# Performance work log

Measured on AMD Instinct MI355X. Metric: run time of the kernel, lower is better.

## Reference

```python
import jax, jax.numpy as jnp
import numpy as np

EPS = 0.05  # blend weight of K_Rectify smoothing


def k_rectify(x_nbc, distance, idx, eps=EPS):
    """Distance-weighted neighbor smoothing.
    x_nbc: (N, B, C); distance, idx: (B, N, K). Returns (N, B, C)."""
    x_bnc = jnp.transpose(x_nbc, (1, 0, 2))                       # (B,N,C)
    B = x_bnc.shape[0]
    neigh = x_bnc[jnp.arange(B)[:, None, None], idx]              # (B,N,K,C) gather
    w = jax.nn.softmax(-distance, axis=-1)                        # closer -> larger weight
    smoothed = jnp.einsum('bnk,bnkc->bnc', w, neigh)              # (B,N,C)
    y = (1.0 - eps) * x_bnc + eps * smoothed
    return jnp.transpose(y, (1, 0, 2))


def monarch_linear(x, w1, w2, bias):
    """Monarch block-diagonal butterfly multiply on the last dim.
    w1: (k,q,p), w2: (l,s,r) with k*p == n, l*r == k*q."""
    shp = x.shape
    k, q, p = w1.shape
    l, s, r = w2.shape
    xb = x.reshape(-1, k, p)
    o1 = jnp.einsum('kqp,bkp->bkq', w1, xb)                       # (B*, k, q)
    o1 = o1.reshape(-1, r, l).transpose(0, 2, 1)                  # 'b (r l) -> b l r'
    o2 = jnp.einsum('lsr,blr->bls', w2, o1)                       # (B*, l, s)
    out = o2.transpose(0, 2, 1).reshape(-1, s * l) + bias         # 'b l s -> b (s l)'
    return out.reshape(*shp[:-1], s * l)


def setup_inputs() -> dict:
    key = jax.random.key(0)
    B, N, C, K, nblocks = 8, 8192, 256, 8, 8
    blk = C // nblocks
    ks = jax.random.split(key, 6)
    x = jax.random.normal(ks[0], (B, N, C), dtype=jnp.float32)
    distance = jax.random.uniform(ks[1], (B, N, K), dtype=jnp.float32)
    idx = jax.random.randint(ks[2], (B, N, K), 0, N)
    rf = jax.random.normal(ks[3], (B, N, C), dtype=jnp.float32)
    scale = 1.0 / np.sqrt(blk)
    w1 = jax.random.normal(ks[4], (nblocks, blk, blk), dtype=jnp.float32) * scale
    w2 = jax.random.normal(ks[5], (nblocks, blk, blk), dtype=jnp.float32) * scale
    bias = jnp.zeros((C,), dtype=jnp.float32)
    return {"x": x, "distance": distance, "idx": idx, "rf": rf,
            "w1": w1, "w2": w2, "bias": bias}


def reference(x, distance, idx, rf, w1, w2, bias):
    # _prepare_in: (B,N,C) -> (N,B,C)
    xs = jnp.transpose(x, (1, 0, 2))
    s1 = k_rectify(xs, distance, idx)            # smooth_in
    t = monarch_linear(s1, w1, w2, bias)         # Monarch block-diag matmul
    s2 = k_rectify(t, distance, idx)             # smooth_out
    return jnp.transpose(s2, (1, 0, 2)) + rf     # _out_transform residual
```

## Files before the change

kernel.cpp:

```cpp
#include <hip/hip_runtime.h>

#define NPTS 8192
#define CH   256
#define KNB  8
#define NROWS 65536
#define ROWS_PER_BLK 32
#define ROWS_PER_IT  4
#define NIT (ROWS_PER_BLK / ROWS_PER_IT)
#define FT_STRIDE 36

#define NBLK_CONV 8192
#define NBLK_S1   (NROWS / ROWS_PER_BLK)
#define NBLK_S2   (NROWS / 16)

typedef unsigned short ushort_t;
typedef float  f32x4  __attribute__((ext_vector_type(4)));

#define BARRIER_LDS() do { \
    asm volatile("s_waitcnt lgkmcnt(0)" ::: "memory"); \
    __builtin_amdgcn_s_barrier(); \
} while (0)

__device__ __forceinline__ int xcd_swz(int h, int cpx) {
    return (h & 7) * cpx + (h >> 3);
}

__device__ __forceinline__ ushort_t f32_to_bf16(float f) {
    unsigned int b = __float_as_uint(f);
    b += 0x7FFFu + ((b >> 16) & 1u);
    return (ushort_t)(b >> 16);
}
__device__ __forceinline__ float bf16_to_f32(ushort_t u) {
    return __uint_as_float(((unsigned int)u) << 16);
}
__device__ __forceinline__ unsigned int pack_bf16(float lo, float hi) {
    return (unsigned int)f32_to_bf16(lo) | ((unsigned int)f32_to_bf16(hi) << 16);
}

__global__ __launch_bounds__(256) void pm_conv(
    const f32x4* __restrict__ x, uint4* __restrict__ xb)
{
    const int l = xcd_swz(blockIdx.x, NBLK_CONV / 8);
    const size_t i = (size_t)l * 256 + threadIdx.x;
    const f32x4 a = __builtin_nontemporal_load(&x[2 * i]);
    const f32x4 c = __builtin_nontemporal_load(&x[2 * i + 1]);
    uint4 o;
    o.x = pack_bf16(a.x, a.y);
    o.y = pack_bf16(a.z, a.w);
    o.z = pack_bf16(c.x, c.y);
    o.w = pack_bf16(c.z, c.w);
    xb[i] = o;
}

__global__ __launch_bounds__(256, 4) void pm_stage1(
    const ushort_t* __restrict__ xb, const float* __restrict__ dist,
    const int* __restrict__ idx, const float* __restrict__ w1,
    const float* __restrict__ w2, const float* __restrict__ bias,
    ushort_t* __restrict__ t)
{
    const int c = threadIdx.x;

    __shared__ float s1[ROWS_PER_IT][CH];
    __shared__ float fT[ROWS_PER_IT][8 * FT_STRIDE];

    float4 w1r[8], w2r[8];
    {
        const float4* w1p = (const float4*)(w1 + c * 32);
        const float4* w2p = (const float4*)(w2 + ((c & 7) * 32 + (c >> 3)) * 32);
#pragma unroll
        for (int i = 0; i < 8; ++i) { w1r[i] = w1p[i]; w2r[i] = w2p[i]; }
    }
    const float bb = bias[c];
    const int l2   = c & 7;
    const int kb   = c >> 5;
    const int ftw  = l2 * FT_STRIDE + (c >> 3);

    const int rr   = __builtin_amdgcn_readfirstlane(threadIdx.x >> 6);
    const int lane = threadIdx.x & 63;

    const int lb       = xcd_swz(blockIdx.x, NBLK_S1 / 8);
    const int row_base = lb * ROWS_PER_BLK;
    const int b = row_base >> 13;
    const char* xbase  = (const char*)(xb + (size_t)b * NPTS * CH);
    const int laneoff  = lane * 8;

    float dcur[KNB]; int nbs[KNB];
    {
        const int row = row_base + rr;
        const float4 d0 = *(const float4*)(dist + (size_t)row * KNB);
        const float4 d1 = *(const float4*)(dist + (size_t)row * KNB + 4);
        const int4   i0 = *(const int4*)(idx + (size_t)row * KNB);
        const int4   i1 = *(const int4*)(idx + (size_t)row * KNB + 4);
        dcur[0]=d0.x; dcur[1]=d0.y; dcur[2]=d0.z; dcur[3]=d0.w;
        dcur[4]=d1.x; dcur[5]=d1.y; dcur[6]=d1.z; dcur[7]=d1.w;
        nbs[0]=__builtin_amdgcn_readfirstlane(i0.x);
        nbs[1]=__builtin_amdgcn_readfirstlane(i0.y);
        nbs[2]=__builtin_amdgcn_readfirstlane(i0.z);
        nbs[3]=__builtin_amdgcn_readfirstlane(i0.w);
        nbs[4]=__builtin_amdgcn_readfirstlane(i1.x);
        nbs[5]=__builtin_amdgcn_readfirstlane(i1.y);
        nbs[6]=__builtin_amdgcn_readfirstlane(i1.z);
        nbs[7]=__builtin_amdgcn_readfirstlane(i1.w);
    }
    ushort4 c0, g[KNB];
    {
        const int rloc = (row_base + rr) & (NPTS - 1);
        c0 = *(const ushort4*)(xbase + ((size_t)rloc << 9) + laneoff);
#pragma unroll
        for (int k = 0; k < KNB; ++k)
            g[k] = *(const ushort4*)(xbase + ((size_t)(unsigned)nbs[k] << 9) + laneoff);
    }

    for (int it = 0; it < NIT; ++it) {
        const bool more = (it + 1 < NIT);
        const int rown  = row_base + (more ? it + 1 : it) * ROWS_PER_IT + rr;

        const float4 dn0 = *(const float4*)(dist + (size_t)rown * KNB);
        const float4 dn1 = *(const float4*)(dist + (size_t)rown * KNB + 4);
        const int4   in0 = *(const int4*)(idx + (size_t)rown * KNB);
        const int4   in1 = *(const int4*)(idx + (size_t)rown * KNB + 4);

        float mn = dcur[0];
#pragma unroll
        for (int k = 1; k < KNB; ++k) mn = fminf(mn, dcur[k]);
        float e[KNB]; float sum = 0.f;
#pragma unroll
        for (int k = 0; k < KNB; ++k) { e[k] = __expf(mn - dcur[k]); sum += e[k]; }
        const float inv = 0.05f / sum;

        float4 acc;
        acc.x = 0.95f * bf16_to_f32(c0.x);
        acc.y = 0.95f * bf16_to_f32(c0.y);
        acc.z = 0.95f * bf16_to_f32(c0.z);
        acc.w = 0.95f * bf16_to_f32(c0.w);
#pragma unroll
        for (int k = 0; k < KNB; ++k) {
            const float w = e[k] * inv;
            acc.x += w * bf16_to_f32(g[k].x);
            acc.y += w * bf16_to_f32(g[k].y);
            acc.z += w * bf16_to_f32(g[k].z);
            acc.w += w * bf16_to_f32(g[k].w);
        }
        ((float4*)&s1[rr][0])[lane] = acc;

        BARRIER_LDS();

#pragma unroll
        for (int r2 = 0; r2 < ROWS_PER_IT; ++r2) {
            const float4* sb = (const float4*)(&s1[r2][kb * 32]);
            float a = 0.f;
#pragma unroll
            for (int p4 = 0; p4 < 8; ++p4) {
                const float4 s = sb[p4];
                a += w1r[p4].x * s.x + w1r[p4].y * s.y
                   + w1r[p4].z * s.z + w1r[p4].w * s.w;
            }
            fT[r2][ftw] = a;
        }

        if (more) {
            dcur[0]=dn0.x; dcur[1]=dn0.y; dcur[2]=dn0.z; dcur[3]=dn0.w;
            dcur[4]=dn1.x; dcur[5]=dn1.y; dcur[6]=dn1.z; dcur[7]=dn1.w;
            nbs[0]=__builtin_amdgcn_readfirstlane(in0.x);
            nbs[1]=__builtin_amdgcn_readfirstlane(in0.y);
            nbs[2]=__builtin_amdgcn_readfirstlane(in0.z);
            nbs[3]=__builtin_amdgcn_readfirstlane(in0.w);
            nbs[4]=__builtin_amdgcn_readfirstlane(in1.x);
            nbs[5]=__builtin_amdgcn_readfirstlane(in1.y);
            nbs[6]=__builtin_amdgcn_readfirstlane(in1.z);
            nbs[7]=__builtin_amdgcn_readfirstlane(in1.w);
            const int rloc = rown & (NPTS - 1);
            c0 = *(const ushort4*)(xbase + ((size_t)rloc << 9) + laneoff);
#pragma unroll
            for (int k = 0; k < KNB; ++k)
                g[k] = *(const ushort4*)(xbase + ((size_t)(unsigned)nbs[k] << 9) + laneoff);
        }

        BARRIER_LDS();

#pragma unroll
        for (int r2 = 0; r2 < ROWS_PER_IT; ++r2) {
            const float4* fp = (const float4*)(&fT[r2][l2 * FT_STRIDE]);
            float a = bb;
#pragma unroll
            for (int r4 = 0; r4 < 8; ++r4) {
                const float4 f = fp[r4];
                a += w2r[r4].x * f.x + w2r[r4].y * f.y
                   + w2r[r4].z * f.z + w2r[r4].w * f.w;
            }
            __builtin_nontemporal_store(
                f32_to_bf16(a),
                &t[(size_t)(row_base + it * ROWS_PER_IT + r2) * CH + c]);
        }
    }
}

__global__ __launch_bounds__(256, 4) void pm_stage2(
    const ushort_t* __restrict__ t, const float* __restrict__ dist,
    const int* __restrict__ idx, const float* __restrict__ rf,
    float* __restrict__ out)
{
    const int w     = __builtin_amdgcn_readfirstlane(threadIdx.x >> 6);
    const int lane  = threadIdx.x & 63;
    const int lb    = xcd_swz(blockIdx.x, NBLK_S2 / 8);
    const int wrow0 = lb * 16 + w * 4;
    const int b     = wrow0 >> 13;
    const char* tbase = (const char*)(t + (size_t)b * NPTS * CH);
    const int laneoff = lane * 8;

    int   nbs[4][KNB];
    float d [4][KNB];
#pragma unroll
    for (int r = 0; r < 4; ++r) {
        const int row = wrow0 + r;
        const float4 d0 = *(const float4*)(dist + (size_t)row * KNB);
        const float4 d1 = *(const float4*)(dist + (size_t)row * KNB + 4);
        const int4   i0 = *(const int4*)(idx + (size_t)row * KNB);
        const int4   i1 = *(const int4*)(idx + (size_t)row * KNB + 4);
        d[r][0]=d0.x; d[r][1]=d0.y; d[r][2]=d0.z; d[r][3]=d0.w;
        d[r][4]=d1.x; d[r][5]=d1.y; d[r][6]=d1.z; d[r][7]=d1.w;
        nbs[r][0]=__builtin_amdgcn_readfirstlane(i0.x);
        nbs[r][1]=__builtin_amdgcn_readfirstlane(i0.y);
        nbs[r][2]=__builtin_amdgcn_readfirstlane(i0.z);
        nbs[r][3]=__builtin_amdgcn_readfirstlane(i0.w);
        nbs[r][4]=__builtin_amdgcn_readfirstlane(i1.x);
        nbs[r][5]=__builtin_amdgcn_readfirstlane(i1.y);
        nbs[r][6]=__builtin_amdgcn_readfirstlane(i1.z);
        nbs[r][7]=__builtin_amdgcn_readfirstlane(i1.w);
    }

    ushort4 c0[4], g[4][KNB];
    f32x4   rv[4];
#pragma unroll
    for (int r = 0; r < 4; ++r) {
        const int rloc = (wrow0 + r) & (NPTS - 1);
        c0[r] = *(const ushort4*)(tbase + ((size_t)rloc << 9) + laneoff);
        rv[r] = __builtin_nontemporal_load(
                    &((const f32x4*)rf)[(size_t)(wrow0 + r) * 64 + lane]);
#pragma unroll
        for (int k = 0; k < KNB; ++k)
            g[r][k] = *(const ushort4*)(tbase + ((size_t)(unsigned)nbs[r][k] << 9) + laneoff);
    }

#pragma unroll
    for (int r = 0; r < 4; ++r) {
        float mn = d[r][0];
#pragma unroll
        for (int k = 1; k < KNB; ++k) mn = fminf(mn, d[r][k]);
        float e[KNB]; float sum = 0.f;
#pragma unroll
        for (int k = 0; k < KNB; ++k) { e[k] = __expf(mn - d[r][k]); sum += e[k]; }
        const float inv = 0.05f / sum;

        f32x4 acc;
        acc.x = 0.95f * bf16_to_f32(c0[r].x) + rv[r].x;
        acc.y = 0.95f * bf16_to_f32(c0[r].y) + rv[r].y;
        acc.z = 0.95f * bf16_to_f32(c0[r].z) + rv[r].z;
        acc.w = 0.95f * bf16_to_f32(c0[r].w) + rv[r].w;
#pragma unroll
        for (int k = 0; k < KNB; ++k) {
            const float wk = e[k] * inv;
            acc.x += wk * bf16_to_f32(g[r][k].x);
            acc.y += wk * bf16_to_f32(g[r][k].y);
            acc.z += wk * bf16_to_f32(g[r][k].z);
            acc.w += wk * bf16_to_f32(g[r][k].w);
        }
        __builtin_nontemporal_store(
            acc, &((f32x4*)out)[(size_t)(wrow0 + r) * 64 + lane]);
    }
}

extern "C" void kernel_launch(void* const* d_in, const int* in_sizes, int n_in,
                              void* d_out, int out_size, void* d_ws, size_t ws_size,
                              hipStream_t stream) {
    const float* x    = (const float*)d_in[0];
    const float* dist = (const float*)d_in[1];
    const int*   idx  = (const int*)d_in[2];
    const float* rf   = (const float*)d_in[3];
    const float* w1   = (const float*)d_in[4];
    const float* w2   = (const float*)d_in[5];
    const float* bias = (const float*)d_in[6];
    float* out = (float*)d_out;

    ushort_t* t  = (ushort_t*)d_ws;
    ushort_t* xb = (ushort_t*)((char*)d_ws + (size_t)NROWS * CH * 2);

    pm_conv  <<<NBLK_CONV, 256, 0, stream>>>((const f32x4*)x, (uint4*)xb);
    pm_stage1<<<NBLK_S1,   256, 0, stream>>>(xb, dist, idx, w1, w2, bias, t);
    pm_stage2<<<NBLK_S2,   256, 0, stream>>>(t, dist, idx, rf, out);
}
```

Measured before the change: 267.0 us.

## Batch stage1 into 16-row phases with double-buffered gathers and transient weight registers

Stage1 now handles 16 rows per barrier phase instead of 4. Two gather buffers are interleaved so neighbour loads for upcoming rows are in flight while the current rows are blended. The Monarch weights are reloaded into registers per phase instead of being held for the whole kernel, which frees VGPRs for the extra in-flight gathers. This cuts barrier count and raises memory-level parallelism, at the cost of repeated weight loads from cache, more LDS, and possible register pressure. The stage2 blend is also rewritten with vector arithmetic.

```diff
diff --git a/kernel.cpp b/kernel.cpp
--- a/kernel.cpp
+++ b/kernel.cpp
@@ -5,8 +5,7 @@
 #define KNB  8
 #define NROWS 65536
 #define ROWS_PER_BLK 32
-#define ROWS_PER_IT  4
-#define NIT (ROWS_PER_BLK / ROWS_PER_IT)
+#define PHASE_ROWS 16
 #define FT_STRIDE 36
 
 #define NBLK_CONV 8192
@@ -35,6 +34,12 @@
 }
 __device__ __forceinline__ unsigned int pack_bf16(float lo, float hi) {
     return (unsigned int)f32_to_bf16(lo) | ((unsigned int)f32_to_bf16(hi) << 16);
+}
+__device__ __forceinline__ f32x4 bf4(ushort4 u) {
+    f32x4 r;
+    r.x = bf16_to_f32(u.x); r.y = bf16_to_f32(u.y);
+    r.z = bf16_to_f32(u.z); r.w = bf16_to_f32(u.w);
+    return r;
 }
 
 __global__ __launch_bounds__(256) void pm_conv(
@@ -60,16 +65,9 @@
 {
     const int c = threadIdx.x;
 
-    __shared__ float s1[ROWS_PER_IT][CH];
-    __shared__ float fT[ROWS_PER_IT][8 * FT_STRIDE];
-
-    float4 w1r[8], w2r[8];
-    {
-        const float4* w1p = (const float4*)(w1 + c * 32);
-        const float4* w2p = (const float4*)(w2 + ((c & 7) * 32 + (c >> 3)) * 32);
-#pragma unroll
-        for (int i = 0; i < 8; ++i) { w1r[i] = w1p[i]; w2r[i] = w2p[i]; }
-    }
+    __shared__ float s1[PHASE_ROWS][CH];
+    __shared__ float fT[PHASE_ROWS][8 * FT_STRIDE];
+
     const float bb = bias[c];
     const int l2   = c & 7;
     const int kb   = c >> 5;
@@ -84,115 +82,112 @@
     const char* xbase  = (const char*)(xb + (size_t)b * NPTS * CH);
     const int laneoff  = lane * 8;
 
-    float dcur[KNB]; int nbs[KNB];
-    {
-        const int row = row_base + rr;
-        const float4 d0 = *(const float4*)(dist + (size_t)row * KNB);
-        const float4 d1 = *(const float4*)(dist + (size_t)row * KNB + 4);
-        const int4   i0 = *(const int4*)(idx + (size_t)row * KNB);
-        const int4   i1 = *(const int4*)(idx + (size_t)row * KNB + 4);
-        dcur[0]=d0.x; dcur[1]=d0.y; dcur[2]=d0.z; dcur[3]=d0.w;
-        dcur[4]=d1.x; dcur[5]=d1.y; dcur[6]=d1.z; dcur[7]=d1.w;
-        nbs[0]=__builtin_amdgcn_readfirstlane(i0.x);
-        nbs[1]=__builtin_amdgcn_readfirstlane(i0.y);
-        nbs[2]=__builtin_amdgcn_readfirstlane(i0.z);
-        nbs[3]=__builtin_amdgcn_readfirstlane(i0.w);
-        nbs[4]=__builtin_amdgcn_readfirstlane(i1.x);
-        nbs[5]=__builtin_amdgcn_readfirstlane(i1.y);
-        nbs[6]=__builtin_amdgcn_readfirstlane(i1.z);
-        nbs[7]=__builtin_amdgcn_readfirstlane(i1.w);
-    }
-    ushort4 c0, g[KNB];
-    {
-        const int rloc = (row_base + rr) & (NPTS - 1);
-        c0 = *(const ushort4*)(xbase + ((size_t)rloc << 9) + laneoff);
-#pragma unroll
-        for (int k = 0; k < KNB; ++k)
-            g[k] = *(const ushort4*)(xbase + ((size_t)(unsigned)nbs[k] << 9) + laneoff);
-    }
-
-    for (int it = 0; it < NIT; ++it) {
-        const bool more = (it + 1 < NIT);
-        const int rown  = row_base + (more ? it + 1 : it) * ROWS_PER_IT + rr;
-
-        const float4 dn0 = *(const float4*)(dist + (size_t)rown * KNB);
-        const float4 dn1 = *(const float4*)(dist + (size_t)rown * KNB + 4);
-        const int4   in0 = *(const int4*)(idx + (size_t)rown * KNB);
-        const int4   in1 = *(const int4*)(idx + (size_t)rown * KNB + 4);
-
-        float mn = dcur[0];
-#pragma unroll
-        for (int k = 1; k < KNB; ++k) mn = fminf(mn, dcur[k]);
-        float e[KNB]; float sum = 0.f;
-#pragma unroll
-        for (int k = 0; k < KNB; ++k) { e[k] = __expf(mn - dcur[k]); sum += e[k]; }
-        const float inv = 0.05f / sum;
-
-        float4 acc;
-        acc.x = 0.95f * bf16_to_f32(c0.x);
-        acc.y = 0.95f * bf16_to_f32(c0.y);
-        acc.z = 0.95f * bf16_to_f32(c0.z);
-        acc.w = 0.95f * bf16_to_f32(c0.w);
-#pragma unroll
-        for (int k = 0; k < KNB; ++k) {
-            const float w = e[k] * inv;
-            acc.x += w * bf16_to_f32(g[k].x);
-            acc.y += w * bf16_to_f32(g[k].y);
-            acc.z += w * bf16_to_f32(g[k].z);
-            acc.w += w * bf16_to_f32(g[k].w);
-        }
-        ((float4*)&s1[rr][0])[lane] = acc;
+#define LOAD_META(dd, nn, row) do {                                        \
+    const float4 m0_ = *(const float4*)(dist + (size_t)(row) * KNB);       \
+    const float4 m1_ = *(const float4*)(dist + (size_t)(row) * KNB + 4);   \
+    const int4   j0_ = *(const int4*)(idx + (size_t)(row) * KNB);          \
+    const int4   j1_ = *(const int4*)(idx + (size_t)(row) * KNB + 4);      \
+    dd[0]=m0_.x; dd[1]=m0_.y; dd[2]=m0_.z; dd[3]=m0_.w;                    \
+    dd[4]=m1_.x; dd[5]=m1_.y; dd[6]=m1_.z; dd[7]=m1_.w;                    \
+    nn[0]=__builtin_amdgcn_readfirstlane(j0_.x);                           \
+    nn[1]=__builtin_amdgcn_readfirstlane(j0_.y);                           \
+    nn[2]=__builtin_amdgcn_readfirstlane(j0_.z);                           \
+    nn[3]=__builtin_amdgcn_readfirstlane(j0_.w);                           \
+    nn[4]=__builtin_amdgcn_readfirstlane(j1_.x);                           \
+    nn[5]=__builtin_amdgcn_readfirstlane(j1_.y);                           \
+    nn[6]=__builtin_amdgcn_readfirstlane(j1_.z);                           \
+    nn[7]=__builtin_amdgcn_readfirstlane(j1_.w);                           \
+} while (0)
+
+#define ISSUE_G(cc, gg, nn, row) do {                                      \
+    const int rloc_ = (row) & (NPTS - 1);                                  \
+    cc = *(const ushort4*)(xbase + ((size_t)rloc_ << 9) + laneoff);        \
+    _Pragma("unroll")                                                      \
+    for (int k_ = 0; k_ < KNB; ++k_)                                       \
+        gg[k_] = *(const ushort4*)(xbase + ((size_t)(unsigned)nn[k_] << 9) + laneoff); \
+} while (0)
+
+#define BLEND(cc, gg, dd, srow) do {                                       \
+    float mn_ = dd[0];                                                     \
+    _Pragma("unroll")                                                      \
+    for (int k_ = 1; k_ < KNB; ++k_) mn_ = fminf(mn_, dd[k_]);             \
+    float e_[KNB]; float sum_ = 0.f;                                       \
+    _Pragma("unroll")                                                      \
+    for (int k_ = 0; k_ < KNB; ++k_) { e_[k_] = __expf(mn_ - dd[k_]); sum_ += e_[k_]; } \
+    const float inv_ = 0.05f / sum_;                                       \
+    f32x4 acc_ = 0.95f * bf4(cc);                                          \
+    _Pragma("unroll")                                                      \
+    for (int k_ = 0; k_ < KNB; ++k_) acc_ += (e_[k_] * inv_) * bf4(gg[k_]); \
+    *(f32x4*)(&s1[srow][lane * 4]) = acc_;                                 \
+} while (0)
+
+    float dA[KNB], dB[KNB];
+    int   nA[KNB], nB[KNB];
+    ushort4 cA, gA[KNB], cB, gB[KNB];
+
+    LOAD_META(dA, nA, row_base + rr);
+    LOAD_META(dB, nB, row_base + 4 + rr);
+    ISSUE_G(cA, gA, nA, row_base + rr);
+    ISSUE_G(cB, gB, nB, row_base + 4 + rr);
+
+#pragma unroll
+    for (int ph = 0; ph < 2; ++ph) {
+        const int prow = row_base + ph * PHASE_ROWS + rr;
+
+        BLEND(cA, gA, dA, 0 * 4 + rr);
+        LOAD_META(dA, nA, prow + 8);  ISSUE_G(cA, gA, nA, prow + 8);
+        BLEND(cB, gB, dB, 1 * 4 + rr);
+        LOAD_META(dB, nB, prow + 12); ISSUE_G(cB, gB, nB, prow + 12);
+        BLEND(cA, gA, dA, 2 * 4 + rr);
+        BLEND(cB, gB, dB, 3 * 4 + rr);
 
         BARRIER_LDS();
 
-#pragma unroll
-        for (int r2 = 0; r2 < ROWS_PER_IT; ++r2) {
-            const float4* sb = (const float4*)(&s1[r2][kb * 32]);
-            float a = 0.f;
-#pragma unroll
-            for (int p4 = 0; p4 < 8; ++p4) {
-                const float4 s = sb[p4];
-                a += w1r[p4].x * s.x + w1r[p4].y * s.y
-                   + w1r[p4].z * s.z + w1r[p4].w * s.w;
-            }
-            fT[r2][ftw] = a;
-        }
-
-        if (more) {
-            dcur[0]=dn0.x; dcur[1]=dn0.y; dcur[2]=dn0.z; dcur[3]=dn0.w;
-            dcur[4]=dn1.x; dcur[5]=dn1.y; dcur[6]=dn1.z; dcur[7]=dn1.w;
-            nbs[0]=__builtin_amdgcn_readfirstlane(in0.x);
-            nbs[1]=__builtin_amdgcn_readfirstlane(in0.y);
-            nbs[2]=__builtin_amdgcn_readfirstlane(in0.z);
-            nbs[3]=__builtin_amdgcn_readfirstlane(in0.w);
-            nbs[4]=__builtin_amdgcn_readfirstlane(in1.x);
-            nbs[5]=__builtin_amdgcn_readfirstlane(in1.y);
-            nbs[6]=__builtin_amdgcn_readfirstlane(in1.z);
-            nbs[7]=__builtin_amdgcn_readfirstlane(in1.w);
-            const int rloc = rown & (NPTS - 1);
-            c0 = *(const ushort4*)(xbase + ((size_t)rloc << 9) + laneoff);
-#pragma unroll
-            for (int k = 0; k < KNB; ++k)
-                g[k] = *(const ushort4*)(xbase + ((size_t)(unsigned)nbs[k] << 9) + laneoff);
+        f32x4 w1r[8];
+        {
+            const f32x4* w1p = (const f32x4*)(w1 + c * 32);
+#pragma unroll
+            for (int i = 0; i < 8; ++i) { w1r[i] = w1p[i]; asm volatile("" : "+v"(w1r[i])); }
+        }
+#pragma unroll
+        for (int r2 = 0; r2 < PHASE_ROWS; ++r2) {
+            const f32x4* sb = (const f32x4*)(&s1[r2][kb * 32]);
+            f32x4 a4 = {0.f, 0.f, 0.f, 0.f};
+#pragma unroll
+            for (int p4 = 0; p4 < 8; ++p4) a4 += w1r[p4] * sb[p4];
+            fT[r2][ftw] = (a4.x + a4.y) + (a4.z + a4.w);
+        }
+
+        if (ph == 0) {
+            LOAD_META(dA, nA, row_base + PHASE_ROWS + rr);
+            ISSUE_G(cA, gA, nA, row_base + PHASE_ROWS + rr);
+            LOAD_META(dB, nB, row_base + PHASE_ROWS + 4 + rr);
+            ISSUE_G(cB, gB, nB, row_base + PHASE_ROWS + 4 + rr);
         }
 
         BARRIER_LDS();
 
-#pragma unroll
-        for (int r2 = 0; r2 < ROWS_PER_IT; ++r2) {
-            const float4* fp = (const float4*)(&fT[r2][l2 * FT_STRIDE]);
-            float a = bb;
-#pragma unroll
-            for (int r4 = 0; r4 < 8; ++r4) {
-                const float4 f = fp[r4];
-                a += w2r[r4].x * f.x + w2r[r4].y * f.y
-                   + w2r[r4].z * f.z + w2r[r4].w * f.w;
-            }
+        f32x4 w2r[8];
+        {
+            const f32x4* w2p = (const f32x4*)(w2 + ((c & 7) * 32 + (c >> 3)) * 32);
+#pragma unroll
+            for (int i = 0; i < 8; ++i) { w2r[i] = w2p[i]; asm volatile("" : "+v"(w2r[i])); }
+        }
+#pragma unroll
+        for (int r2 = 0; r2 < PHASE_ROWS; ++r2) {
+            const f32x4* fp = (const f32x4*)(&fT[r2][l2 * FT_STRIDE]);
+            f32x4 a4 = {0.f, 0.f, 0.f, 0.f};
+#pragma unroll
+            for (int r4 = 0; r4 < 8; ++r4) a4 += w2r[r4] * fp[r4];
+            const float a = bb + ((a4.x + a4.y) + (a4.z + a4.w));
             __builtin_nontemporal_store(
                 f32_to_bf16(a),
-                &t[(size_t)(row_base + it * ROWS_PER_IT + r2) * CH + c]);
-        }
-    }
+                &t[(size_t)(row_base + ph * PHASE_ROWS + r2) * CH + c]);
+        }
+    }
+#undef LOAD_META
+#undef ISSUE_G
+#undef BLEND
 }
 
 __global__ __launch_bounds__(256, 4) void pm_stage2(
@@ -252,19 +247,10 @@
         for (int k = 0; k < KNB; ++k) { e[k] = __expf(mn - d[r][k]); sum += e[k]; }
         const float inv = 0.05f / sum;
 
-        f32x4 acc;
-        acc.x = 0.95f * bf16_to_f32(c0[r].x) + rv[r].x;
-        acc.y = 0.95f * bf16_to_f32(c0[r].y) + rv[r].y;
-        acc.z = 0.95f * bf16_to_f32(c0[r].z) + rv[r].z;
-        acc.w = 0.95f * bf16_to_f32(c0[r].w) + rv[r].w;
-#pragma unroll
-        for (int k = 0; k < KNB; ++k) {
-            const float wk = e[k] * inv;
-            acc.x += wk * bf16_to_f32(g[r][k].x);
-            acc.y += wk * bf16_to_f32(g[r][k].y);
-            acc.z += wk * bf16_to_f32(g[r][k].z);
-            acc.w += wk * bf16_to_f32(g[r][k].w);
-        }
+        f32x4 acc = 0.95f * bf4(c0[r]) + rv[r];
+#pragma unroll
+        for (int k = 0; k < KNB; ++k)
+            acc += (e[k] * inv) * bf4(g[r][k]);
         __builtin_nontemporal_store(
             acc, &((f32x4*)out)[(size_t)(wrow0 + r) * 64 + lane]);
     }
```

Result: slower. 280.7 us (+5.1%).

## Overlap neighbor gather with first Monarch GEMM and vectorize FMA chains

Applied to the files above, without the earlier changes.

Stage 1 now issues the next row's neighbor gathers before the barrier and runs the first block-diagonal multiply after that barrier, alongside the second multiply. The goal is to overlap gather latency with compute. Both multiplies and the smoothing loops use ext-vector f32x4 arithmetic with four independent partial sums, which shortens dependency chains and may allow packed FMA. An asm barrier keeps the weights pinned in VGPRs, and launch bounds are relaxed from 4 to 3 waves to leave room for more registers, at some cost in occupancy.

```diff
diff --git a/kernel.cpp b/kernel.cpp
--- a/kernel.cpp
+++ b/kernel.cpp
@@ -35,6 +35,12 @@
 }
 __device__ __forceinline__ unsigned int pack_bf16(float lo, float hi) {
     return (unsigned int)f32_to_bf16(lo) | ((unsigned int)f32_to_bf16(hi) << 16);
+}
+__device__ __forceinline__ f32x4 bf4(ushort4 u) {
+    f32x4 r;
+    r.x = bf16_to_f32(u.x); r.y = bf16_to_f32(u.y);
+    r.z = bf16_to_f32(u.z); r.w = bf16_to_f32(u.w);
+    return r;
 }
 
 __global__ __launch_bounds__(256) void pm_conv(
@@ -52,7 +58,7 @@
     xb[i] = o;
 }
 
-__global__ __launch_bounds__(256, 4) void pm_stage1(
+__global__ __launch_bounds__(256, 3) void pm_stage1(
     const ushort_t* __restrict__ xb, const float* __restrict__ dist,
     const int* __restrict__ idx, const float* __restrict__ w1,
     const float* __restrict__ w2, const float* __restrict__ bias,
@@ -63,12 +69,15 @@
     __shared__ float s1[ROWS_PER_IT][CH];
     __shared__ float fT[ROWS_PER_IT][8 * FT_STRIDE];
 
-    float4 w1r[8], w2r[8];
+    f32x4 w1r[8], w2r[8];
     {
-        const float4* w1p = (const float4*)(w1 + c * 32);
-        const float4* w2p = (const float4*)(w2 + ((c & 7) * 32 + (c >> 3)) * 32);
-#pragma unroll
-        for (int i = 0; i < 8; ++i) { w1r[i] = w1p[i]; w2r[i] = w2p[i]; }
+        const f32x4* w1p = (const f32x4*)(w1 + c * 32);
+        const f32x4* w2p = (const f32x4*)(w2 + ((c & 7) * 32 + (c >> 3)) * 32);
+#pragma unroll
+        for (int i = 0; i < 8; ++i) {
+            w1r[i] = w1p[i]; w2r[i] = w2p[i];
+            asm volatile("" : "+v"(w1r[i]), "+v"(w2r[i]));
+        }
     }
     const float bb = bias[c];
     const int l2   = c & 7;
@@ -128,35 +137,10 @@
         for (int k = 0; k < KNB; ++k) { e[k] = __expf(mn - dcur[k]); sum += e[k]; }
         const float inv = 0.05f / sum;
 
-        float4 acc;
-        acc.x = 0.95f * bf16_to_f32(c0.x);
-        acc.y = 0.95f * bf16_to_f32(c0.y);
-        acc.z = 0.95f * bf16_to_f32(c0.z);
-        acc.w = 0.95f * bf16_to_f32(c0.w);
-#pragma unroll
-        for (int k = 0; k < KNB; ++k) {
-            const float w = e[k] * inv;
-            acc.x += w * bf16_to_f32(g[k].x);
-            acc.y += w * bf16_to_f32(g[k].y);
-            acc.z += w * bf16_to_f32(g[k].z);
-            acc.w += w * bf16_to_f32(g[k].w);
-        }
-        ((float4*)&s1[rr][0])[lane] = acc;
-
-        BARRIER_LDS();
-
-#pragma unroll
-        for (int r2 = 0; r2 < ROWS_PER_IT; ++r2) {
-            const float4* sb = (const float4*)(&s1[r2][kb * 32]);
-            float a = 0.f;
-#pragma unroll
-            for (int p4 = 0; p4 < 8; ++p4) {
-                const float4 s = sb[p4];
-                a += w1r[p4].x * s.x + w1r[p4].y * s.y
-                   + w1r[p4].z * s.z + w1r[p4].w * s.w;
-            }
-            fT[r2][ftw] = a;
-        }
+        f32x4 acc = 0.95f * bf4(c0);
+#pragma unroll
+        for (int k = 0; k < KNB; ++k) acc += (e[k] * inv) * bf4(g[k]);
+        *(f32x4*)(&s1[rr][lane * 4]) = acc;
 
         if (more) {
             dcur[0]=dn0.x; dcur[1]=dn0.y; dcur[2]=dn0.z; dcur[3]=dn0.w;
@@ -180,14 +164,22 @@
 
 #pragma unroll
         for (int r2 = 0; r2 < ROWS_PER_IT; ++r2) {
-            const float4* fp = (const float4*)(&fT[r2][l2 * FT_STRIDE]);
-            float a = bb;
-#pragma unroll
-            for (int r4 = 0; r4 < 8; ++r4) {
-                const float4 f = fp[r4];
-                a += w2r[r4].x * f.x + w2r[r4].y * f.y
-                   + w2r[r4].z * f.z + w2r[r4].w * f.w;
-            }
+            const f32x4* sb = (const f32x4*)(&s1[r2][kb * 32]);
+            f32x4 a4 = {0.f, 0.f, 0.f, 0.f};
+#pragma unroll
+            for (int p4 = 0; p4 < 8; ++p4) a4 += w1r[p4] * sb[p4];
+            fT[r2][ftw] = (a4.x + a4.y) + (a4.z + a4.w);
+        }
+
+        BARRIER_LDS();
+
+#pragma unroll
+        for (int r2 = 0; r2 < ROWS_PER_IT; ++r2) {
+            const f32x4* fp = (const f32x4*)(&fT[r2][l2 * FT_STRIDE]);
+            f32x4 a4 = {0.f, 0.f, 0.f, 0.f};
+#pragma unroll
+            for (int r4 = 0; r4 < 8; ++r4) a4 += w2r[r4] * fp[r4];
+            const float a = bb + ((a4.x + a4.y) + (a4.z + a4.w));
             __builtin_nontemporal_store(
                 f32_to_bf16(a),
                 &t[(size_t)(row_base + it * ROWS_PER_IT + r2) * CH + c]);
@@ -252,19 +244,10 @@
         for (int k = 0; k < KNB; ++k) { e[k] = __expf(mn - d[r][k]); sum += e[k]; }
         const float inv = 0.05f / sum;
 
-        f32x4 acc;
-        acc.x = 0.95f * bf16_to_f32(c0[r].x) + rv[r].x;
-        acc.y = 0.95f * bf16_to_f32(c0[r].y) + rv[r].y;
-        acc.z = 0.95f * bf16_to_f32(c0[r].z) + rv[r].z;
-        acc.w = 0.95f * bf16_to_f32(c0[r].w) + rv[r].w;
-#pragma unroll
-        for (int k = 0; k < KNB; ++k) {
-            const float wk = e[k] * inv;
-            acc.x += wk * bf16_to_f32(g[r][k].x);
-            acc.y += wk * bf16_to_f32(g[r][k].y);
-            acc.z += wk * bf16_to_f32(g[r][k].z);
-            acc.w += wk * bf16_to_f32(g[r][k].w);
-        }
+        f32x4 acc = 0.95f * bf4(c0[r]) + rv[r];
+#pragma unroll
+        for (int k = 0; k < KNB; ++k)
+            acc += (e[k] * inv) * bf4(g[r][k]);
         __builtin_nontemporal_store(
             acc, &((f32x4*)out)[(size_t)(wrow0 + r) * 64 + lane]);
     }
```

Result: slower. 274.1 us (+2.7%).
